# Kernel optimization log

Hardware: AMD Instinct MI355X
Metric: run time of the kernel (lower is better)

## Reference

```python
import jax, jax.numpy as jnp
import numpy as np


def setup_inputs() -> dict:
    key = jax.random.key(0)
    k1, k2, k3, k4 = jax.random.split(key, 4)
    B, N, F, S, OUT = 8, 50000, 32, 16, 64
    x = jax.random.normal(k1, (B, N, F), dtype=jnp.float32)
    spiral_adj = jax.random.randint(k2, (B, N, S), 0, N, dtype=jnp.int64)
    W = jax.random.normal(k3, (OUT, F * S), dtype=jnp.float32) * (1.0 / np.sqrt(F * S))
    b = jax.random.normal(k4, (OUT,), dtype=jnp.float32) * 0.01
    return {"x": x, "spiral_adj": spiral_adj, "W": W, "b": b}


def reference(x, spiral_adj, W, b):
    B, N, F = x.shape
    S = spiral_adj.shape[-1]
    # Per-batch gather of spiral neighbors: (B, N, S, F)
    spirals = jax.vmap(lambda xb, ab: xb[ab])(x, spiral_adj)
    spirals = spirals.reshape(B, N, S * F)
    # Linear: y = spirals @ W^T + b, then ELU
    out = jnp.einsum('bnk,ok->bno', spirals, W) + b
    out = jax.nn.elu(out)
    # zero out the last (padding) vertex
    mask = jnp.ones((1, N, 1), dtype=out.dtype).at[0, -1, 0].set(0.0)
    return out * mask
```

## Files before the change

kernel.cpp:

```cpp
#include <hip/hip_runtime.h>
#include <hip/hip_bf16.h>
#include <string.h>

#define B_ 8
#define N_ 50000
#define F_ 32
#define S_ 16
#define O_ 64
#define K_ (F_ * S_)
#define NTILES ((B_ * N_) / 16)
#define XELEMS (B_ * N_ * F_)

typedef __attribute__((ext_vector_type(8))) short bf16x8;
typedef __attribute__((ext_vector_type(4))) float f32x4;

union bfpack { bf16x8 v; __hip_bfloat16 h[8]; };

__global__ __launch_bounds__(256) void prep_kernel(const float* __restrict__ W,
                                                   unsigned short* __restrict__ Wb,
                                                   const float* __restrict__ x,
                                                   unsigned short* __restrict__ xb) {
    int bid = blockIdx.x;
    if (bid < 128) {
        int i = bid * 256 + threadIdx.x;
        int j = i & 7;
        int o = (i >> 3) & 63;
        int qk = i >> 9;
        int quad = qk & 3;
        int kt = qk >> 2;
        __hip_bfloat16 h = __float2bfloat16(W[o * K_ + kt * 32 + quad * 8 + j]);
        unsigned short u; memcpy(&u, &h, 2);
        Wb[i] = u;
    } else {
        int i = (bid - 128) * 256 + threadIdx.x;
        if (i < XELEMS / 8) {
            size_t base = (size_t)i * 8;
            f32x4 a = *(const f32x4*)(x + base);
            f32x4 b = *(const f32x4*)(x + base + 4);
            bfpack p;
            p.h[0] = __float2bfloat16(a[0]); p.h[1] = __float2bfloat16(a[1]);
            p.h[2] = __float2bfloat16(a[2]); p.h[3] = __float2bfloat16(a[3]);
            p.h[4] = __float2bfloat16(b[0]); p.h[5] = __float2bfloat16(b[1]);
            p.h[6] = __float2bfloat16(b[2]); p.h[7] = __float2bfloat16(b[3]);
            *(bf16x8*)(xb + base) = p.v;
        }
    }
}

__global__ __launch_bounds__(256) void spiral_kernel(
        const unsigned short* __restrict__ xb, const int* __restrict__ adj,
        const unsigned short* __restrict__ Wb, const float* __restrict__ bias,
        float* __restrict__ out) {
    const int lane = threadIdx.x & 63;
    const int wv   = threadIdx.x >> 6;
    const int m16  = lane & 15;
    const int quad = lane >> 4;

    const int tile0 = (blockIdx.x * 4 + wv) * 4;

    int rowbase[4];
    int nn[4], bb[4];
#pragma unroll
    for (int vt = 0; vt < 4; ++vt) {
        int t = tile0 + vt;
        if (t >= NTILES) t = NTILES - 1;
        int g = t * 16;
        int bi = g / N_;
        bb[vt] = bi;
        nn[vt] = g - bi * N_;
        rowbase[vt] = g;
    }

    f32x4 acc[4][4];
#pragma unroll
    for (int vt = 0; vt < 4; ++vt)
#pragma unroll
        for (int nt = 0; nt < 4; ++nt)
            acc[vt][nt] = (f32x4){0.f, 0.f, 0.f, 0.f};

#pragma unroll
    for (int kt4 = 0; kt4 < 4; ++kt4) {
        int4 aj[4];
#pragma unroll
        for (int vt = 0; vt < 4; ++vt)
            aj[vt] = *(const int4*)(adj + (size_t)(rowbase[vt] + m16) * S_ + kt4 * 4);

#pragma unroll
        for (int q = 0; q < 4; ++q) {
            const int kt = kt4 * 4 + q;
            bf16x8 xf[4];
#pragma unroll
            for (int vt = 0; vt < 4; ++vt) {
                int a = ((const int*)&aj[vt])[q];
                xf[vt] = *(const bf16x8*)(xb + (size_t)(bb[vt] * N_ + a) * F_ + quad * 8);
            }
            bf16x8 wf[4];
#pragma unroll
            for (int nt = 0; nt < 4; ++nt)
                wf[nt] = *(const bf16x8*)(Wb + (size_t)((kt * 4 + quad) * 64 + nt * 16 + m16) * 8);
#pragma unroll
            for (int vt = 0; vt < 4; ++vt)
#pragma unroll
                for (int nt = 0; nt < 4; ++nt)
                    acc[vt][nt] = __builtin_amdgcn_mfma_f32_16x16x32_bf16(wf[nt], xf[vt], acc[vt][nt], 0, 0, 0);
        }
    }

#pragma unroll
    for (int vt = 0; vt < 4; ++vt) {
        const int n = nn[vt] + m16;
        const bool zero = (n == N_ - 1);
        float* orow = out + (size_t)(rowbase[vt] + m16) * O_ + quad * 4;
#pragma unroll
        for (int nt = 0; nt < 4; ++nt) {
            f32x4 bv = *(const f32x4*)(bias + nt * 16 + quad * 4);
            f32x4 v;
#pragma unroll
            for (int r = 0; r < 4; ++r) {
                float t = acc[vt][nt][r] + bv[r];
                t = t > 0.f ? t : (__expf(t) - 1.f);
                v[r] = zero ? 0.f : t;
            }
            *(f32x4*)(orow + nt * 16) = v;
        }
    }
}

__global__ __launch_bounds__(256) void wconv_kernel(const float* __restrict__ W,
                                                    unsigned short* __restrict__ Wb) {
    int i = blockIdx.x * 256 + threadIdx.x;
    if (i < O_ * K_) {
        int j = i & 7, o = (i >> 3) & 63, qk = i >> 9;
        int quad = qk & 3, kt = qk >> 2;
        __hip_bfloat16 h = __float2bfloat16(W[o * K_ + kt * 32 + quad * 8 + j]);
        unsigned short u; memcpy(&u, &h, 2);
        Wb[i] = u;
    }
}

__global__ __launch_bounds__(256) void spiral_f32_kernel(
        const float* __restrict__ x, const int* __restrict__ adj,
        const unsigned short* __restrict__ Wb, const float* __restrict__ bias,
        float* __restrict__ out) {
    const int lane = threadIdx.x & 63;
    const int wv = threadIdx.x >> 6;
    const int m16 = lane & 15, quad = lane >> 4;
    const int tile0 = (blockIdx.x * 4 + wv) * 4;
    int bb[4], nn[4];
#pragma unroll
    for (int vt = 0; vt < 4; ++vt) {
        int t = tile0 + vt;
        if (t >= NTILES) t = NTILES - 1;
        int g = t * 16, bi = g / N_;
        bb[vt] = bi; nn[vt] = g - bi * N_;
    }
    f32x4 acc[4][4];
#pragma unroll
    for (int vt = 0; vt < 4; ++vt)
#pragma unroll
        for (int nt = 0; nt < 4; ++nt) acc[vt][nt] = (f32x4){0.f,0.f,0.f,0.f};
    for (int kt = 0; kt < 16; ++kt) {
        bf16x8 wf[4];
#pragma unroll
        for (int nt = 0; nt < 4; ++nt)
            wf[nt] = *(const bf16x8*)(Wb + (size_t)((kt * 4 + quad) * 64 + nt * 16 + m16) * 8);
#pragma unroll
        for (int vt = 0; vt < 4; ++vt) {
            int n = nn[vt] + m16;
            int a = adj[(size_t)(bb[vt] * N_ + n) * S_ + kt];
            const float* xr = x + (size_t)(bb[vt] * N_ + a) * F_ + quad * 8;
            f32x4 x0 = *(const f32x4*)xr;
            f32x4 x1 = *(const f32x4*)(xr + 4);
            bfpack af;
            af.h[0]=__float2bfloat16(x0[0]); af.h[1]=__float2bfloat16(x0[1]);
            af.h[2]=__float2bfloat16(x0[2]); af.h[3]=__float2bfloat16(x0[3]);
            af.h[4]=__float2bfloat16(x1[0]); af.h[5]=__float2bfloat16(x1[1]);
            af.h[6]=__float2bfloat16(x1[2]); af.h[7]=__float2bfloat16(x1[3]);
#pragma unroll
            for (int nt = 0; nt < 4; ++nt)
                acc[vt][nt] = __builtin_amdgcn_mfma_f32_16x16x32_bf16(wf[nt], af.v, acc[vt][nt], 0, 0, 0);
        }
    }
#pragma unroll
    for (int vt = 0; vt < 4; ++vt) {
        const int n = nn[vt] + m16;
        const bool zero = (n == N_ - 1);
        float* orow = out + (size_t)(bb[vt] * N_ + n) * O_ + quad * 4;
#pragma unroll
        for (int nt = 0; nt < 4; ++nt) {
            f32x4 bv = *(const f32x4*)(bias + nt * 16 + quad * 4);
            f32x4 v;
#pragma unroll
            for (int r = 0; r < 4; ++r) {
                float t = acc[vt][nt][r] + bv[r];
                t = t > 0.f ? t : (__expf(t) - 1.f);
                v[r] = zero ? 0.f : t;
            }
            *(f32x4*)(orow + nt * 16) = v;
        }
    }
}

extern "C" void kernel_launch(void* const* d_in, const int* in_sizes, int n_in,
                              void* d_out, int out_size, void* d_ws, size_t ws_size,
                              hipStream_t stream) {
    const float* x    = (const float*)d_in[0];
    const int*   adj  = (const int*)d_in[1];
    const float* W    = (const float*)d_in[2];
    const float* bias = (const float*)d_in[3];
    float* out = (float*)d_out;

    const size_t wb_bytes = (size_t)O_ * K_ * 2;
    const size_t xb_bytes = (size_t)XELEMS * 2;
    unsigned short* Wb = (unsigned short*)d_ws;
    unsigned short* xb = (unsigned short*)((char*)d_ws + wb_bytes);

    const int grid_main = (NTILES + 15) / 16;

    if (ws_size >= wb_bytes + xb_bytes) {
        int grid_prep = 128 + (XELEMS / 8 + 255) / 256;
        hipLaunchKernelGGL(prep_kernel, dim3(grid_prep), dim3(256), 0, stream, W, Wb, x, xb);
        hipLaunchKernelGGL(spiral_kernel, dim3(grid_main), dim3(256), 0, stream,
                           xb, adj, Wb, bias, out);
    } else {
        hipLaunchKernelGGL(wconv_kernel, dim3(128), dim3(256), 0, stream, W, Wb);
        hipLaunchKernelGGL(spiral_f32_kernel, dim3(grid_main), dim3(256), 0, stream,
                           x, adj, Wb, bias, out);
    }
}
```

Measured before the change: 260.5 us.

## Interleave batches across consecutive blocks and use nontemporal loads in prep

```diff
diff --git a/kernel.cpp b/kernel.cpp
--- a/kernel.cpp
+++ b/kernel.cpp
@@ -8,8 +8,9 @@
 #define S_ 16
 #define O_ 64
 #define K_ (F_ * S_)
-#define NTILES ((B_ * N_) / 16)
 #define XELEMS (B_ * N_ * F_)
+#define TPB (N_ / 16)
+#define BPB 196
 
 typedef __attribute__((ext_vector_type(8))) short bf16x8;
 typedef __attribute__((ext_vector_type(4))) float f32x4;
@@ -35,8 +36,8 @@
         int i = (bid - 128) * 256 + threadIdx.x;
         if (i < XELEMS / 8) {
             size_t base = (size_t)i * 8;
-            f32x4 a = *(const f32x4*)(x + base);
-            f32x4 b = *(const f32x4*)(x + base + 4);
+            f32x4 a = __builtin_nontemporal_load((const f32x4*)(x + base));
+            f32x4 b = __builtin_nontemporal_load((const f32x4*)(x + base + 4));
             bfpack p;
             p.h[0] = __float2bfloat16(a[0]); p.h[1] = __float2bfloat16(a[1]);
             p.h[2] = __float2bfloat16(a[2]); p.h[3] = __float2bfloat16(a[3]);
@@ -56,20 +57,20 @@
     const int m16  = lane & 15;
     const int quad = lane >> 4;
 
-    const int tile0 = (blockIdx.x * 4 + wv) * 4;
+    const int b  = blockIdx.x & 7;
+    const int jb = blockIdx.x >> 3;
+    const int tib0 = (jb * 4 + wv) * 4;
 
     int rowbase[4];
-    int nn[4], bb[4];
-#pragma unroll
-    for (int vt = 0; vt < 4; ++vt) {
-        int t = tile0 + vt;
-        if (t >= NTILES) t = NTILES - 1;
-        int g = t * 16;
-        int bi = g / N_;
-        bb[vt] = bi;
-        nn[vt] = g - bi * N_;
-        rowbase[vt] = g;
-    }
+    int nn[4];
+#pragma unroll
+    for (int vt = 0; vt < 4; ++vt) {
+        int t = tib0 + vt;
+        if (t >= TPB) t = TPB - 1;
+        nn[vt] = t * 16;
+        rowbase[vt] = b * N_ + t * 16;
+    }
+    const size_t xbase = (size_t)b * N_ * F_;
 
     f32x4 acc[4][4];
 #pragma unroll
@@ -92,7 +93,7 @@
 #pragma unroll
             for (int vt = 0; vt < 4; ++vt) {
                 int a = ((const int*)&aj[vt])[q];
-                xf[vt] = *(const bf16x8*)(xb + (size_t)(bb[vt] * N_ + a) * F_ + quad * 8);
+                xf[vt] = *(const bf16x8*)(xb + xbase + (size_t)a * F_ + quad * 8);
             }
             bf16x8 wf[4];
 #pragma unroll
@@ -145,14 +146,16 @@
     const int lane = threadIdx.x & 63;
     const int wv = threadIdx.x >> 6;
     const int m16 = lane & 15, quad = lane >> 4;
-    const int tile0 = (blockIdx.x * 4 + wv) * 4;
-    int bb[4], nn[4];
-#pragma unroll
-    for (int vt = 0; vt < 4; ++vt) {
-        int t = tile0 + vt;
-        if (t >= NTILES) t = NTILES - 1;
-        int g = t * 16, bi = g / N_;
-        bb[vt] = bi; nn[vt] = g - bi * N_;
+    const int b  = blockIdx.x & 7;
+    const int jb = blockIdx.x >> 3;
+    const int tib0 = (jb * 4 + wv) * 4;
+    int rowbase[4], nn[4];
+#pragma unroll
+    for (int vt = 0; vt < 4; ++vt) {
+        int t = tib0 + vt;
+        if (t >= TPB) t = TPB - 1;
+        nn[vt] = t * 16;
+        rowbase[vt] = b * N_ + t * 16;
     }
     f32x4 acc[4][4];
 #pragma unroll
@@ -166,9 +169,8 @@
             wf[nt] = *(const bf16x8*)(Wb + (size_t)((kt * 4 + quad) * 64 + nt * 16 + m16) * 8);
 #pragma unroll
         for (int vt = 0; vt < 4; ++vt) {
-            int n = nn[vt] + m16;
-            int a = adj[(size_t)(bb[vt] * N_ + n) * S_ + kt];
-            const float* xr = x + (size_t)(bb[vt] * N_ + a) * F_ + quad * 8;
+            int a = adj[(size_t)(rowbase[vt] + m16) * S_ + kt];
+            const float* xr = x + ((size_t)b * N_ + a) * F_ + quad * 8;
             f32x4 x0 = *(const f32x4*)xr;
             f32x4 x1 = *(const f32x4*)(xr + 4);
             bfpack af;
@@ -185,7 +187,7 @@
     for (int vt = 0; vt < 4; ++vt) {
         const int n = nn[vt] + m16;
         const bool zero = (n == N_ - 1);
-        float* orow = out + (size_t)(bb[vt] * N_ + n) * O_ + quad * 4;
+        float* orow = out + (size_t)(rowbase[vt] + m16) * O_ + quad * 4;
 #pragma unroll
         for (int nt = 0; nt < 4; ++nt) {
             f32x4 bv = *(const f32x4*)(bias + nt * 16 + quad * 4);
@@ -215,7 +217,7 @@
     unsigned short* Wb = (unsigned short*)d_ws;
     unsigned short* xb = (unsigned short*)((char*)d_ws + wb_bytes);
 
-    const int grid_main = (NTILES + 15) / 16;
+    const int grid_main = 8 * BPB;
 
     if (ws_size >= wb_bytes + xb_bytes) {
         int grid_prep = 128 + (XELEMS / 8 + 255) / 256;
```

New measurement: 237.1 us. -9.0%, faster.
